# Kernel tuning notes

Measured on AMD Instinct MI355X. Metric: run time of the kernel, lower is better.

Reference implementation:

```python
import jax, jax.numpy as jnp
import numpy as np

B, T, C, H, N = 2, 1024, 2048, 32, 64  # batch, seq, n_embd==dim_att, heads, head_size
EPS_GN = 64e-5  # torch GroupNorm eps=0.00064


def setup_inputs() -> dict:
    key = jax.random.key(0)
    ks = jax.random.split(key, 40)
    def rn(i, shape, s):
        return jax.random.normal(ks[i], shape, dtype=jnp.float32) * s
    return {
        'x': jax.random.normal(ks[0], (B, T, C), dtype=jnp.float32),
        'shift_state': jnp.zeros((B, C), jnp.float32),
        'wkv_state': jnp.zeros((B, H, N, N), jnp.float32),
        'time_maa_x': rn(1, (1, 1, C), 0.3),
        'time_maa_rg': rn(2, (1, 1, C), 0.3),
        'time_maa_wa': rn(3, (1, 1, C), 0.3),
        'time_maa_k': rn(4, (1, 1, C), 0.3),
        'time_maa_v': rn(5, (1, 1, C), 0.3),
        'time_maa_w1': rn(6, (C, 128), 0.02),   # D_MIX_LORA*4 = 128
        'time_maa_w2': rn(7, (4, 32, C), 0.02),
        'time_decay': rn(8, (1, 1, C), 0.5) - 4.0,
        'time_decay_w1': rn(9, (C, 64), 0.02),
        'time_decay_w2': rn(10, (64, C), 0.02),
        'time_faaaa': rn(11, (1, 1, H, N), 0.02),
        'time_aaaaa': rn(12, (1, 1, C), 0.02),
        'time_aaa_w1': rn(13, (C, 16), 0.02),
        'time_aaa_w2': rn(14, (16, C), 0.02),
        'time_kkk_w1': rn(15, (C, 16), 0.02),
        'time_kkk_w2': rn(16, (16, C), 0.02),
        'gate_w1': rn(17, (C, 128), 0.02),
        'gate_w2': rn(18, (128, C), 0.02),
        'ma_w1': rn(19, (C, 16), 0.02),
        'ma_w2': rn(20, (16, C), 0.02),
        'time_misc_a': rn(21, (1, 1, C), 0.02),
        'mk_w1': rn(22, (C, 16), 0.02),
        'mk_w2': rn(23, (16, C), 0.02),
        'time_misc_k': rn(24, (1, 1, C), 0.02),
        'Wr': rn(25, (C, C), 0.5 / np.sqrt(C)),
        'Wk': rn(26, (C, C), 0.05 / np.sqrt(C)),
        'Wv': rn(27, (C, C), 0.5 / np.sqrt(C)),
        'Wo': rn(28, (C, C), 0.5 / np.sqrt(C)),
        'ln_w': jnp.ones((C,), jnp.float32),
        'ln_b': jnp.zeros((C,), jnp.float32),
    }


def _forward(x, shift_state, wkv_state, time_maa_x, time_maa_rg, time_maa_wa,
             time_maa_k, time_maa_v, time_maa_w1, time_maa_w2, time_decay,
             time_decay_w1, time_decay_w2, time_faaaa, time_aaaaa, time_aaa_w1,
             time_aaa_w2, time_kkk_w1, time_kkk_w2, gate_w1, gate_w2, ma_w1,
             ma_w2, time_misc_a, mk_w1, mk_w2, time_misc_k, Wr, Wk, Wv, Wo,
             ln_w, ln_b):
    # token shift difference
    xx = jnp.concatenate([shift_state[:, None, :], x[:, :-1]], axis=1) - x
    xmx = x + xx * time_maa_x
    m = jnp.tanh(xmx @ time_maa_w1).reshape(B, T, 4, -1)   # [B,T,4,32]
    m = jnp.einsum('btfd,fdc->fbtc', m, time_maa_w2)       # [4,B,T,C]
    mrg, mwa, mkm, mv = m[0], m[1], m[2], m[3]
    xrg = x + xx * (time_maa_rg + mrg)
    xwa = x + xx * (time_maa_wa + mwa)
    xk = x + xx * (time_maa_k + mkm)
    xv = x + xx * (time_maa_v + mv)
    r = xrg @ Wr.T
    w = -jax.nn.softplus(-(time_decay + jnp.tanh(xwa @ time_decay_w1) @ time_decay_w2)) - 0.5
    k = xk @ Wk.T
    v = xv @ Wv.T
    g = jnp.tanh(xrg @ gate_w1) @ gate_w2
    kk = k + jnp.tanh(xk @ time_kkk_w1) @ time_kkk_w2
    kkh = kk.reshape(B, T, H, N)
    nrm = jnp.maximum(jnp.linalg.norm(kkh, axis=-1, keepdims=True), 1e-12)  # F.normalize
    kk = (kkh / nrm).reshape(B, T, C)
    a = jax.nn.sigmoid(time_aaaaa + xwa @ time_aaa_w1 @ time_aaa_w2)
    ma = jax.nn.sigmoid(time_misc_a + xwa @ ma_w1 @ ma_w2)
    k = k * ma + k * a * (1.0 - ma)
    mk = jax.nn.sigmoid(time_misc_k + xk @ mk_w1 @ mk_w2)
    k = k * jnp.exp(jnp.minimum(w * mk, 0.0))  # clamp(w*mk, max=0).exp()

    # RWKV-7 recurrence (fused_recurrent_rwkv7 with a=-kk, b=kk*a_gate):
    #   S_t = diag(exp(w_t)) S_{t-1} + b_t (a_t^T S_{t-1}) + k_t v_t^T,  o_t = S_t^T r_t
    def heads(t):
        return jnp.moveaxis(t.reshape(B, T, H, N), 1, 0)  # [T,B,H,N]
    rs, ksq, vs, ws = heads(r), heads(k), heads(v), heads(w)
    a_s, b_s = heads(-kk), heads(kk * a)

    def step(S, inputs):  # S: [B,H,N_key,N_val]
        r_t, k_t, v_t, w_t, a_t, b_t = inputs
        sa = jnp.einsum('bhk,bhkv->bhv', a_t, S)
        S = S * jnp.exp(w_t)[..., None] + k_t[..., None] * v_t[..., None, :] + b_t[..., None] * sa[..., None, :]
        o = jnp.einsum('bhk,bhkv->bhv', r_t, S)
        return S, o

    S_final, o = jax.lax.scan(step, wkv_state, (rs, ksq, vs, ws, a_s, b_s))
    out = jnp.moveaxis(o, 0, 1).reshape(B, T, C)

    # GroupNorm(n_head groups, eps=64e-5), biased variance per head
    y = out.reshape(B * T, H, N)
    mu = y.mean(-1, keepdims=True)
    var = ((y - mu) ** 2).mean(-1, keepdims=True)
    y = (y - mu) / jnp.sqrt(var + EPS_GN)
    y = y * ln_w.reshape(H, N) + ln_b.reshape(H, N)
    xo = y.reshape(B, T, C)

    rh = r.reshape(B, T, H, N)
    kh = k.reshape(B, T, H, N)
    vh = v.reshape(B, T, H, N)
    xo = xo + ((rh * kh * time_faaaa).sum(-1, keepdims=True) * vh).reshape(B, T, C)
    xo = (xo * g) @ Wo.T
    return xo, x[:, -1], S_final


def reference(x, shift_state, wkv_state, time_maa_x, time_maa_rg, time_maa_wa,
              time_maa_k, time_maa_v, time_maa_w1, time_maa_w2, time_decay,
              time_decay_w1, time_decay_w2, time_faaaa, time_aaaaa, time_aaa_w1,
              time_aaa_w2, time_kkk_w1, time_kkk_w2, gate_w1, gate_w2, ma_w1,
              ma_w2, time_misc_a, mk_w1, mk_w2, time_misc_k, Wr, Wk, Wv, Wo,
              ln_w, ln_b):
    return _forward(x, shift_state, wkv_state, time_maa_x, time_maa_rg, time_maa_wa,
                    time_maa_k, time_maa_v, time_maa_w1, time_maa_w2, time_decay,
                    time_decay_w1, time_decay_w2, time_faaaa, time_aaaaa, time_aaa_w1,
                    time_aaa_w2, time_kkk_w1, time_kkk_w2, gate_w1, gate_w2, ma_w1,
                    ma_w2, time_misc_a, mk_w1, mk_w2, time_misc_k, Wr, Wk, Wv, Wo,
                    ln_w, ln_b)
```

## Files before the change

kernel.cpp:

```cpp
#include <hip/hip_runtime.h>
#include <hip/hip_bf16.h>
#include <math.h>


#define B_ 2
#define T_ 1024
#define C_ 2048
#define H_ 32
#define BT_ (B_*T_)
#define BTC_ ((size_t)BT_*C_)
#define CC_ ((size_t)C_*C_)
#define KS_ 8
#define CH_ 8

typedef __bf16 bf16x8 __attribute__((ext_vector_type(8)));
typedef float f32x4 __attribute__((ext_vector_type(4)));

__device__ __forceinline__ float wave64_sum(float v){
#pragma unroll
  for (int d = 1; d < 64; d <<= 1) v += __shfl_xor(v, d, 64);
  return v;
}

__device__ __forceinline__ float dpp_add_xor1(float x){
  int j = __builtin_amdgcn_mov_dpp(__float_as_int(x), 0xB1, 0xF, 0xF, true);
  return x + __int_as_float(j);
}
__device__ __forceinline__ float dpp_add_xor2(float x){
  int j = __builtin_amdgcn_mov_dpp(__float_as_int(x), 0x4E, 0xF, 0xF, true);
  return x + __int_as_float(j);
}
__device__ __forceinline__ float dpp_add_hmir(float x){
  int j = __builtin_amdgcn_mov_dpp(__float_as_int(x), 0x141, 0xF, 0xF, true);
  return x + __int_as_float(j);
}
__device__ __forceinline__ float dpp_add_mir(float x){
  int j = __builtin_amdgcn_mov_dpp(__float_as_int(x), 0x140, 0xF, 0xF, true);
  return x + __int_as_float(j);
}

__device__ __forceinline__ float red16(float x){
  x = dpp_add_xor1(x);
  x = dpp_add_xor2(x);
  x = dpp_add_hmir(x);
  x = dpp_add_mir(x);
  return x;
}

__device__ __forceinline__ size_t bhtn_idx(int r, int c){
  return (((size_t)(r >> 10)*H_ + (c >> 6))*T_ + (r & 1023))*64 + (c & 63);
}

__device__ __forceinline__ void gload_lds16(const float* g, float* l){
  __builtin_amdgcn_global_load_lds((const __attribute__((address_space(1))) void*)g,
                                   (__attribute__((address_space(3))) void*)l, 16, 0, 0);
}
__device__ __forceinline__ void gload_lds16b(const __hip_bfloat16* g, __bf16* l){
  __builtin_amdgcn_global_load_lds((const __attribute__((address_space(1))) void*)g,
                                   (__attribute__((address_space(3))) void*)l, 16, 0, 0);
}

__global__ __launch_bounds__(256) void f2bf_kernel(const float* __restrict__ in,
                                                   __hip_bfloat16* __restrict__ out, size_t n){
  size_t i = (size_t)blockIdx.x*256 + threadIdx.x;
  if (i < n) out[i] = __float2bfloat16(in[i]);
}

__global__ __launch_bounds__(256) void shift_kernel(const float* __restrict__ x,
                                                    const float* __restrict__ shift,
                                                    const float* __restrict__ maa_x,
                                                    float* __restrict__ xx, __hip_bfloat16* __restrict__ xmx_h){
  size_t idx = (size_t)blockIdx.x*256 + threadIdx.x;
  int c = (int)(idx % C_);
  size_t bt = idx / C_;
  int t = (int)(bt % T_);
  int b = (int)(bt / T_);
  float xv = x[idx];
  float prev = (t == 0) ? shift[(size_t)b*C_ + c] : x[idx - C_];
  float d = prev - xv;
  xx[idx] = d;
  xmx_h[idx] = __float2bfloat16(xv + d * maa_x[c]);
}

__global__ __launch_bounds__(256) void tp_pack(const float* __restrict__ in, __hip_bfloat16* __restrict__ out,
                                               int Nsrc, int row_off){
  __shared__ float tile[32][33];
  const int t = threadIdx.x;
  const int k0 = blockIdx.x*32, n0 = blockIdx.y*32;
  const int tn = t & 31, tk = t >> 5;
#pragma unroll
  for (int q = 0; q < 4; q++){
    int ki = tk + 8*q;
    float v = (n0 + tn < Nsrc) ? in[(size_t)(k0+ki)*Nsrc + n0 + tn] : 0.f;
    tile[tn][ki] = v;
  }
  __syncthreads();
#pragma unroll
  for (int q = 0; q < 4; q++){
    int no = tk + 8*q;
    if (n0 + no < Nsrc)
      out[(size_t)(row_off + n0 + no)*2048 + k0 + tn] = __float2bfloat16(tile[no][tn]);
  }
}

__global__ __launch_bounds__(256) void gemm_sk(const __hip_bfloat16* __restrict__ Ah,
                                               const __hip_bfloat16* __restrict__ Bh,
                                               float* __restrict__ parts, int K, int KC){
  __shared__ __bf16 As[128*32];
  __shared__ __bf16 Bs[128*32];
  const int tid = threadIdx.x;
  const int bm = blockIdx.x*128;
  const int z = blockIdx.y;
  const int wid = tid >> 6, lane = tid & 63;
  const int wr = (wid >> 1)*64, wc = (wid & 1)*64;
  const int fr = lane & 15, kg = lane >> 4;
  const int srow = tid >> 2, sk = (tid & 3)*8;
  __bf16* lA = As + wid*512;
  __bf16* lB = Bs + wid*512;
  f32x4 acc[4][4] = {};
  const int kend = z*KC + KC;
  for (int kt = z*KC; kt < kend; kt += 32){
    __syncthreads();
    gload_lds16b(Ah + (size_t)(bm+srow)*K + kt + sk,    lA);
    gload_lds16b(Ah + (size_t)(bm+srow+64)*K + kt + sk, lA + 64*32);
    gload_lds16b(Bh + (size_t)(srow)*K + kt + sk,       lB);
    gload_lds16b(Bh + (size_t)(srow+64)*K + kt + sk,    lB + 64*32);
    __builtin_amdgcn_s_waitcnt(0x3F70);
    __syncthreads();
    bf16x8 af[4], bfr[4];
#pragma unroll
    for (int i = 0; i < 4; i++){
      af[i]  = *(const bf16x8*)(As + (wr + i*16 + fr)*32 + kg*8);
      bfr[i] = *(const bf16x8*)(Bs + (wc + i*16 + fr)*32 + kg*8);
    }
#pragma unroll
    for (int mi = 0; mi < 4; mi++)
#pragma unroll
      for (int ni = 0; ni < 4; ni++)
        acc[mi][ni] = __builtin_amdgcn_mfma_f32_16x16x32_bf16(af[mi], bfr[ni], acc[mi][ni], 0, 0, 0);
  }
  float* Cc = parts + (size_t)z*BT_*128;
  const int orow0 = bm + wr + kg*4;
  const int ocol0 = wc + fr;
#pragma unroll
  for (int mi = 0; mi < 4; mi++)
#pragma unroll
    for (int ni = 0; ni < 4; ni++)
#pragma unroll
      for (int j = 0; j < 4; j++)
        Cc[(size_t)(orow0 + mi*16 + j)*128 + ocol0 + ni*16] = acc[mi][ni][j];
}

__global__ __launch_bounds__(256) void reduce_sk(const float* __restrict__ parts, float* __restrict__ out,
                                                 int tanh_lo, int tanh_hi){
  size_t idx = (size_t)blockIdx.x*256 + threadIdx.x;
  float s = 0.f;
#pragma unroll
  for (int z = 0; z < KS_; z++) s += parts[(size_t)z*BT_*128 + idx];
  int c = (int)(idx & 127);
  if (c >= tanh_lo && c < tanh_hi) s = tanhf(s);
  out[idx] = s;
}

__global__ __launch_bounds__(256) void mm_sk_g(const float* __restrict__ A, const float* __restrict__ W,
                                               __hip_bfloat16* __restrict__ out, int K){
  const int j = blockIdx.y*256 + threadIdx.x;
  const int i0 = blockIdx.x*8;
  float acc[8] = {0,0,0,0,0,0,0,0};
  for (int k = 0; k < K; k++){
    float wv = W[(size_t)k*C_ + j];
#pragma unroll
    for (int r = 0; r < 8; r++) acc[r] += A[(size_t)(i0+r)*K + k] * wv;
  }
#pragma unroll
  for (int r = 0; r < 8; r++) out[(size_t)(i0+r)*C_ + j] = __float2bfloat16(acc[r]);
}

__global__ __launch_bounds__(256) void mix_kernel(
    const float* __restrict__ m1, const float* __restrict__ w2,
    const float* __restrict__ x, const float* __restrict__ xx,
    const float* __restrict__ maa_rg, const float* __restrict__ maa_wa,
    const float* __restrict__ maa_k, const float* __restrict__ maa_v,
    __hip_bfloat16* __restrict__ xrg_h, __hip_bfloat16* __restrict__ xwa_h,
    __hip_bfloat16* __restrict__ xk_h, __hip_bfloat16* __restrict__ xv_h)
{
  const int j = blockIdx.y*256 + threadIdx.x;
  const int i0 = blockIdx.x*8;
  float acc[4][8] = {};
#pragma unroll
  for (int f = 0; f < 4; f++){
    for (int d = 0; d < 32; d++){
      float wv = w2[((size_t)f*32 + d)*C_ + j];
#pragma unroll
      for (int r = 0; r < 8; r++)
        acc[f][r] += m1[(size_t)(i0+r)*128 + f*32 + d] * wv;
    }
  }
  float mrg_ = maa_rg[j], mwa_ = maa_wa[j], mk_ = maa_k[j], mv_ = maa_v[j];
#pragma unroll
  for (int r = 0; r < 8; r++){
    size_t idx = (size_t)(i0+r)*C_ + j;
    float xval = x[idx], xxv = xx[idx];
    xrg_h[idx] = __float2bfloat16(xval + xxv*(mrg_ + acc[0][r]));
    xwa_h[idx] = __float2bfloat16(xval + xxv*(mwa_ + acc[1][r]));
    xk_h[idx]  = __float2bfloat16(xval + xxv*(mk_  + acc[2][r]));
    xv_h[idx]  = __float2bfloat16(xval + xxv*(mv_  + acc[3][r]));
  }
}

__global__ __launch_bounds__(256) void gemm_bt(const __hip_bfloat16* __restrict__ Ah,
                                               const __hip_bfloat16* __restrict__ Bh,
                                               float* __restrict__ Cc, int M, int Nn, int K){
  __shared__ __bf16 As[128*32];
  __shared__ __bf16 Bs[128*32];
  const int tid = threadIdx.x;
  const int bm = blockIdx.x*128, bn = blockIdx.y*128;
  const int wid = tid >> 6, lane = tid & 63;
  const int wr = (wid >> 1)*64, wc = (wid & 1)*64;
  const int fr = lane & 15, kg = lane >> 4;
  const int srow = tid >> 2, sk = (tid & 3)*8;
  __bf16* lA = As + wid*512;
  __bf16* lB = Bs + wid*512;
  f32x4 acc[4][4] = {};
  for (int kt = 0; kt < K; kt += 32){
    __syncthreads();
    gload_lds16b(Ah + (size_t)(bm+srow)*K + kt + sk,    lA);
    gload_lds16b(Ah + (size_t)(bm+srow+64)*K + kt + sk, lA + 64*32);
    gload_lds16b(Bh + (size_t)(bn+srow)*K + kt + sk,    lB);
    gload_lds16b(Bh + (size_t)(bn+srow+64)*K + kt + sk, lB + 64*32);
    __builtin_amdgcn_s_waitcnt(0x3F70);
    __syncthreads();
    bf16x8 af[4], bfr[4];
#pragma unroll
    for (int i = 0; i < 4; i++){
      af[i]  = *(const bf16x8*)(As + (wr + i*16 + fr)*32 + kg*8);
      bfr[i] = *(const bf16x8*)(Bs + (wc + i*16 + fr)*32 + kg*8);
    }
#pragma unroll
    for (int mi = 0; mi < 4; mi++)
#pragma unroll
      for (int ni = 0; ni < 4; ni++)
        acc[mi][ni] = __builtin_amdgcn_mfma_f32_16x16x32_bf16(af[mi], bfr[ni], acc[mi][ni], 0, 0, 0);
  }
  const int orow0 = bm + wr + kg*4;
  const int ocol0 = bn + wc + fr;
#pragma unroll
  for (int mi = 0; mi < 4; mi++)
#pragma unroll
    for (int ni = 0; ni < 4; ni++)
#pragma unroll
      for (int j = 0; j < 4; j++)
        Cc[(size_t)(orow0 + mi*16 + j)*Nn + ocol0 + ni*16] = acc[mi][ni][j];
}

__global__ __launch_bounds__(256) void gemm_bt_T(const __hip_bfloat16* __restrict__ Ah,
                                                 const __hip_bfloat16* __restrict__ Bh,
                                                 float* __restrict__ Cc, int K){
  __shared__ __bf16 As[128*32];
  __shared__ __bf16 Bs[128*32];
  const int tid = threadIdx.x;
  const int bm = blockIdx.x*128, bn = blockIdx.y*128;
  const int wid = tid >> 6, lane = tid & 63;
  const int wr = (wid >> 1)*64, wc = (wid & 1)*64;
  const int fr = lane & 15, kg = lane >> 4;
  const int srow = tid >> 2, sk = (tid & 3)*8;
  __bf16* lA = As + wid*512;
  __bf16* lB = Bs + wid*512;
  f32x4 acc[4][4] = {};
  for (int kt = 0; kt < K; kt += 32){
    __syncthreads();
    gload_lds16b(Ah + (size_t)(bm+srow)*K + kt + sk,    lA);
    gload_lds16b(Ah + (size_t)(bm+srow+64)*K + kt + sk, lA + 64*32);
    gload_lds16b(Bh + (size_t)(bn+srow)*K + kt + sk,    lB);
    gload_lds16b(Bh + (size_t)(bn+srow+64)*K + kt + sk, lB + 64*32);
    __builtin_amdgcn_s_waitcnt(0x3F70);
    __syncthreads();
    bf16x8 af[4], bfr[4];
#pragma unroll
    for (int i = 0; i < 4; i++){
      af[i]  = *(const bf16x8*)(As + (wr + i*16 + fr)*32 + kg*8);
      bfr[i] = *(const bf16x8*)(Bs + (wc + i*16 + fr)*32 + kg*8);
    }
#pragma unroll
    for (int mi = 0; mi < 4; mi++)
#pragma unroll
      for (int ni = 0; ni < 4; ni++)
        acc[mi][ni] = __builtin_amdgcn_mfma_f32_16x16x32_bf16(af[mi], bfr[ni], acc[mi][ni], 0, 0, 0);
  }
  const int r0 = bm + wr + kg*4;
  const int c0 = bn + wc + fr;
#pragma unroll
  for (int mi = 0; mi < 4; mi++)
#pragma unroll
    for (int ni = 0; ni < 4; ni++)
#pragma unroll
      for (int j = 0; j < 4; j++)
        Cc[bhtn_idx(r0 + mi*16 + j, c0 + ni*16)] = acc[mi][ni][j];
}

__global__ __launch_bounds__(256) void lora2_kernel(
    const float* __restrict__ wa1, const float* __restrict__ k1c,
    const float* __restrict__ dw2, const float* __restrict__ aw2, const float* __restrict__ maw2,
    const float* __restrict__ mkw2, const float* __restrict__ kkw2,
    const float* __restrict__ td, const float* __restrict__ aaaaa,
    const float* __restrict__ misc_a, const float* __restrict__ misc_k,
    float* __restrict__ k0, float* __restrict__ a_out,
    float* __restrict__ ew_out, float* __restrict__ kk0_out)
{
  const int j = blockIdx.y*256 + threadIdx.x;
  const int i0 = blockIdx.x*8;
  float accW[8] = {}, accA[8] = {}, accMA[8] = {}, accMK[8] = {}, accKK[8] = {};
  for (int k = 0; k < 64; k++){
    float wv = dw2[(size_t)k*C_ + j];
#pragma unroll
    for (int r = 0; r < 8; r++) accW[r] += wa1[(size_t)(i0+r)*128 + k] * wv;
  }
  for (int k = 0; k < 16; k++){
    float w_a  = aw2[(size_t)k*C_ + j];
    float w_ma = maw2[(size_t)k*C_ + j];
    float w_mk = mkw2[(size_t)k*C_ + j];
    float w_kk = kkw2[(size_t)k*C_ + j];
#pragma unroll
    for (int r = 0; r < 8; r++){
      accA[r]  += wa1[(size_t)(i0+r)*128 + 64 + k] * w_a;
      accMA[r] += wa1[(size_t)(i0+r)*128 + 80 + k] * w_ma;
      accKK[r] += k1c[(size_t)(i0+r)*128 + k] * w_kk;
      accMK[r] += k1c[(size_t)(i0+r)*128 + 16 + k] * w_mk;
    }
  }
  float tdv = td[j], aav = aaaaa[j], mav = misc_a[j], mkv = misc_k[j];
#pragma unroll
  for (int r = 0; r < 8; r++){
    size_t idx = bhtn_idx(i0+r, j);
    float u  = tdv + accW[r];
    float w  = -log1pf(expf(-u)) - 0.5f;
    float a  = 1.f/(1.f + expf(-(aav + accA[r])));
    float ma = 1.f/(1.f + expf(-(mav + accMA[r])));
    float mk = 1.f/(1.f + expf(-(mkv + accMK[r])));
    float kv = k0[idx];
    kk0_out[idx] = kv + accKK[r];
    float kn = kv * (ma + a*(1.f - ma)) * expf(fminf(w*mk, 0.f));
    k0[idx] = kn;
    a_out[idx] = a;
    ew_out[idx] = expf(w);
  }
}

__global__ __launch_bounds__(256) void kknorm_kernel(float* __restrict__ kk0, float* __restrict__ a_bs){
  const size_t grp = (size_t)blockIdx.x*4 + (threadIdx.x >> 6);
  const int lane = threadIdx.x & 63;
  const size_t idx = grp*64 + lane;
  float kv = kk0[idx];
  float ss = wave64_sum(kv*kv);
  float nrm = fmaxf(sqrtf(ss), 1e-12f);
  float kkn = kv / nrm;
  kk0[idx] = kkn;
  a_bs[idx] = kkn * a_bs[idx];
}

__global__ __launch_bounds__(64, 1) void rec_kernel(
    const float* __restrict__ rr, const float* __restrict__ kx,
    const float* __restrict__ vx, const float* __restrict__ ew,
    const float* __restrict__ kkv, const float* __restrict__ bsv,
    const float* __restrict__ s0, float* __restrict__ o, float* __restrict__ sT)
{
  __shared__ __align__(16) float lds[2][6][CH_*64];
  const int g = blockIdx.x;
  const int bh = g & 63;
  const int vg = g >> 6;
  const int b = bh >> 5, h = bh & 31;
  const int lane = threadIdx.x;
  const int cf = lane >> 4;
  const int kq = lane & 15;
  const int k0 = kq*4;
  const int v = vg*4 + cf;

  float S0, S1, S2, S3;
  {
    const float* p = s0 + ((size_t)bh*64 + k0)*64 + v;
    S0 = p[0]; S1 = p[64]; S2 = p[128]; S3 = p[192];
  }

  const size_t sb = (size_t)bh*T_*64;
  const float* g0 = kkv + sb;
  const float* g1 = ew  + sb;
  const float* g2 = kx  + sb;
  const float* g3 = bsv + sb;
  const float* g4 = rr  + sb;
  const float* g5 = vx  + sb;
  float* ob = o + (size_t)b*T_*C_ + h*64 + v;

#define STAGE(c, buf) do{ \
    const size_t co_ = (size_t)(c)*(CH_*64) + lane*4; \
    _Pragma("unroll") \
    for (int j_ = 0; j_ < 2; j_++){ \
      gload_lds16(g0 + co_ + j_*256, &lds[buf][0][j_*256]); \
      gload_lds16(g1 + co_ + j_*256, &lds[buf][1][j_*256]); \
      gload_lds16(g2 + co_ + j_*256, &lds[buf][2][j_*256]); \
      gload_lds16(g3 + co_ + j_*256, &lds[buf][3][j_*256]); \
      gload_lds16(g4 + co_ + j_*256, &lds[buf][4][j_*256]); \
      gload_lds16(g5 + co_ + j_*256, &lds[buf][5][j_*256]); \
    } }while(0)

  STAGE(0, 0);
  const int NCH = T_/CH_;
  for (int c = 0; c < NCH; c++){
    const int cn = (c+1 < NCH) ? c+1 : c;
    STAGE(cn, (c+1)&1);
    __builtin_amdgcn_s_waitcnt(0x0F7C);
    __builtin_amdgcn_sched_barrier(0);
    const int buf = c & 1;
#pragma unroll
    for (int s = 0; s < CH_; s++){
      const int so = s*64 + k0;
      const float4 A  = *(const float4*)(&lds[buf][0][so]);
      const float4 E  = *(const float4*)(&lds[buf][1][so]);
      const float4 Kk = *(const float4*)(&lds[buf][2][so]);
      const float4 Bv = *(const float4*)(&lds[buf][3][so]);
      const float4 R  = *(const float4*)(&lds[buf][4][so]);
      const float vt  = lds[buf][5][s*64 + v];
      float p = (A.x*S0 + A.y*S1) + (A.z*S2 + A.w*S3);
      p = red16(p);
      S0 = S0*E.x + Kk.x*vt - Bv.x*p;
      S1 = S1*E.y + Kk.y*vt - Bv.y*p;
      S2 = S2*E.z + Kk.z*vt - Bv.z*p;
      S3 = S3*E.w + Kk.w*vt - Bv.w*p;
      float op = (R.x*S0 + R.y*S1) + (R.z*S2 + R.w*S3);
      op = red16(op);
      if (kq == 0)
        ob[(size_t)(c*CH_ + s)*C_] = op;
    }
  }
#undef STAGE
  float* pT = sT + ((size_t)bh*64 + k0)*64 + v;
  pT[0] = S0; pT[64] = S1; pT[128] = S2; pT[192] = S3;
}

__global__ __launch_bounds__(256) void post_kernel(
    const float* __restrict__ o, const float* __restrict__ r, const float* __restrict__ k,
    const float* __restrict__ v, const __hip_bfloat16* __restrict__ g,
    const float* __restrict__ lnw, const float* __restrict__ lnb,
    const float* __restrict__ faaaa, __hip_bfloat16* __restrict__ z_h)
{
  const size_t grp = (size_t)blockIdx.x*4 + (threadIdx.x >> 6);
  const int lane = threadIdx.x & 63;
  const int h = (int)(grp & (H_-1));
  const int bt = (int)(grp >> 5);
  const size_t idx  = grp*64 + lane;
  const size_t idx2 = (((size_t)(bt >> 10)*H_ + h)*T_ + (bt & 1023))*64 + lane;
  const int ci = h*64 + lane;
  float y = o[idx];
  float mu = wave64_sum(y) * (1.f/64.f);
  float d = y - mu;
  float var = wave64_sum(d*d) * (1.f/64.f);
  float yn = d * rsqrtf(var + 64e-5f) * lnw[ci] + lnb[ci];
  float s = wave64_sum(r[idx2]*k[idx2]*faaaa[ci]);
  float xo = yn + s*v[idx2];
  z_h[idx] = __float2bfloat16(xo * __bfloat162float(g[idx]));
}

__global__ __launch_bounds__(256) void lastx_kernel(const float* __restrict__ x, float* __restrict__ out1){
  int idx = blockIdx.x*256 + threadIdx.x;
  int b = idx / C_, c = idx % C_;
  out1[idx] = x[((size_t)b*T_ + (T_-1))*C_ + c];
}

extern "C" void kernel_launch(void* const* d_in, const int* in_sizes, int n_in,
                              void* d_out, int out_size, void* d_ws, size_t ws_size,
                              hipStream_t stream){
  (void)in_sizes; (void)n_in; (void)out_size;
  const float* x      = (const float*)d_in[0];
  const float* shift  = (const float*)d_in[1];
  const float* wkv0   = (const float*)d_in[2];
  const float* maa_x  = (const float*)d_in[3];
  const float* maa_rg = (const float*)d_in[4];
  const float* maa_wa = (const float*)d_in[5];
  const float* maa_k  = (const float*)d_in[6];
  const float* maa_v  = (const float*)d_in[7];
  const float* maa_w1 = (const float*)d_in[8];
  const float* maa_w2 = (const float*)d_in[9];
  const float* tdecay = (const float*)d_in[10];
  const float* dw1    = (const float*)d_in[11];
  const float* dw2    = (const float*)d_in[12];
  const float* faaaa  = (const float*)d_in[13];
  const float* aaaaa  = (const float*)d_in[14];
  const float* aw1    = (const float*)d_in[15];
  const float* aw2    = (const float*)d_in[16];
  const float* kkw1   = (const float*)d_in[17];
  const float* kkw2   = (const float*)d_in[18];
  const float* gw1    = (const float*)d_in[19];
  const float* gw2    = (const float*)d_in[20];
  const float* maw1   = (const float*)d_in[21];
  const float* maw2   = (const float*)d_in[22];
  const float* misc_a = (const float*)d_in[23];
  const float* mkw1   = (const float*)d_in[24];
  const float* mkw2   = (const float*)d_in[25];
  const float* misc_k = (const float*)d_in[26];
  const float* Wr     = (const float*)d_in[27];
  const float* Wk     = (const float*)d_in[28];
  const float* Wv     = (const float*)d_in[29];
  const float* Wo     = (const float*)d_in[30];
  const float* lnw    = (const float*)d_in[31];
  const float* lnb    = (const float*)d_in[32];

  float* out0 = (float*)d_out;
  float* out1 = out0 + BTC_;
  float* outS = out1 + (size_t)B_*C_;

  const size_t NEEDED = (6*BTC_ + (size_t)3*BT_*128)*4 + 5*CC_*2 + (size_t)4*128*2048*2;
  if (ws_size < NEEDED) return;

  float* ws = (float*)d_ws;
  float* rbuf  = ws;
  float* kbuf  = ws + 1*BTC_;
  float* vbuf  = ws + 2*BTC_;
  float* abuf  = ws + 3*BTC_;
  float* ewbuf = ws + 4*BTC_;
  float* kkbuf = ws + 5*BTC_;
  float* xx    = abuf;
  float* wa1   = ws + 6*BTC_;
  float* g1f   = wa1 + (size_t)BT_*128;
  float* k1c   = g1f + (size_t)BT_*128;
  float* parts = rbuf;
  float* m1f   = vbuf;
  __hip_bfloat16* hb = (__hip_bfloat16*)(k1c + (size_t)BT_*128);
  __hip_bfloat16* xrg_h = hb;
  __hip_bfloat16* xwa_h = hb + 1*CC_;
  __hip_bfloat16* xk_h  = hb + 2*CC_;
  __hip_bfloat16* xv_h  = hb + 3*CC_;
  __hip_bfloat16* Wb    = hb + 4*CC_;
  __hip_bfloat16* WtB   = hb + 5*CC_;
  __hip_bfloat16* Wt_m  = WtB;
  __hip_bfloat16* Wt_wa = WtB + (size_t)128*2048;
  __hip_bfloat16* Wt_g  = WtB + (size_t)2*128*2048;
  __hip_bfloat16* Wt_k  = WtB + (size_t)3*128*2048;
  __hip_bfloat16* xmx_h = xv_h;
  __hip_bfloat16* g_h   = xwa_h;
  __hip_bfloat16* z_h   = xv_h;
  __hip_bfloat16* Wk_h  = (__hip_bfloat16*)ewbuf;
  __hip_bfloat16* Wv_h  = (__hip_bfloat16*)kkbuf;

  dim3 blk(256);
  const int KC = C_/KS_;

  hipMemsetAsync(WtB, 0, (size_t)4*128*2048*2, stream);
  tp_pack<<<dim3(64,4), blk, 0, stream>>>(maa_w1, Wt_m, 128, 0);
  tp_pack<<<dim3(64,2), blk, 0, stream>>>(dw1,  Wt_wa, 64, 0);
  tp_pack<<<dim3(64,1), blk, 0, stream>>>(aw1,  Wt_wa, 16, 64);
  tp_pack<<<dim3(64,1), blk, 0, stream>>>(maw1, Wt_wa, 16, 80);
  tp_pack<<<dim3(64,4), blk, 0, stream>>>(gw1,  Wt_g, 128, 0);
  tp_pack<<<dim3(64,1), blk, 0, stream>>>(kkw1, Wt_k, 16, 0);
  tp_pack<<<dim3(64,1), blk, 0, stream>>>(mkw1, Wt_k, 16, 16);

  shift_kernel<<<(int)(BTC_/256), blk, 0, stream>>>(x, shift, maa_x, xx, xmx_h);

  gemm_sk<<<dim3(BT_/128, KS_), blk, 0, stream>>>(xmx_h, Wt_m, parts, C_, KC);
  reduce_sk<<<BT_*128/256, blk, 0, stream>>>(parts, m1f, 0, 128);

  mix_kernel<<<dim3(BT_/8, C_/256), blk, 0, stream>>>(m1f, maa_w2, x, xx, maa_rg, maa_wa, maa_k, maa_v,
                                                      xrg_h, xwa_h, xk_h, xv_h);
  gemm_sk<<<dim3(BT_/128, KS_), blk, 0, stream>>>(xwa_h, Wt_wa, parts, C_, KC);
  reduce_sk<<<BT_*128/256, blk, 0, stream>>>(parts, wa1, 0, 64);
  gemm_sk<<<dim3(BT_/128, KS_), blk, 0, stream>>>(xrg_h, Wt_g, parts, C_, KC);
  reduce_sk<<<BT_*128/256, blk, 0, stream>>>(parts, g1f, 0, 128);
  gemm_sk<<<dim3(BT_/128, KS_), blk, 0, stream>>>(xk_h, Wt_k, parts, C_, KC);
  reduce_sk<<<BT_*128/256, blk, 0, stream>>>(parts, k1c, 0, 16);

  mm_sk_g<<<dim3(BT_/8, C_/256), blk, 0, stream>>>(g1f, gw2, g_h, 128);

  f2bf_kernel<<<(int)(CC_/256), blk, 0, stream>>>(Wr, Wb, CC_);
  f2bf_kernel<<<(int)(CC_/256), blk, 0, stream>>>(Wk, Wk_h, CC_);
  f2bf_kernel<<<(int)(CC_/256), blk, 0, stream>>>(Wv, Wv_h, CC_);
  gemm_bt_T<<<dim3(BT_/128, C_/128), blk, 0, stream>>>(xrg_h, Wb,   rbuf, C_);
  gemm_bt_T<<<dim3(BT_/128, C_/128), blk, 0, stream>>>(xk_h,  Wk_h, kbuf, C_);
  gemm_bt_T<<<dim3(BT_/128, C_/128), blk, 0, stream>>>(xv_h,  Wv_h, vbuf, C_);

  lora2_kernel<<<dim3(BT_/8, C_/256), blk, 0, stream>>>(wa1, k1c,
                                                        dw2, aw2, maw2, mkw2, kkw2,
                                                        tdecay, aaaaa, misc_a, misc_k,
                                                        kbuf, abuf, ewbuf, kkbuf);
  kknorm_kernel<<<BT_*H_/4, blk, 0, stream>>>(kkbuf, abuf);

  rec_kernel<<<1024, dim3(64), 0, stream>>>(rbuf, kbuf, vbuf, ewbuf, kkbuf, abuf, wkv0, out0, outS);

  post_kernel<<<BT_*H_/4, blk, 0, stream>>>(out0, rbuf, kbuf, vbuf, g_h, lnw, lnb, faaaa, z_h);
  f2bf_kernel<<<(int)(CC_/256), blk, 0, stream>>>(Wo, Wb, CC_);
  gemm_bt<<<dim3(BT_/128, C_/128), blk, 0, stream>>>(z_h, Wb, out0, BT_, C_, C_);
  lastx_kernel<<<(B_*C_)/256, blk, 0, stream>>>(x, out1);
}
```

Measured before the change: 862.6 us.

## Double-buffer LDS in GEMM kernels and batch r/k/v projections into one launch

The three MFMA GEMM kernels now use two LDS buffers, so the global-to-LDS load for the next K-tile is issued before the MFMAs on the current tile. This replaces two barriers per iteration with one, letting memory latency overlap compute. The three separate r/k/v projection GEMMs are merged into one launch that uses blockIdx.z to pick operands, which triples the grid and improves occupancy across CUs. In exchange LDS use doubles to 32KB per block, which may lower resident blocks per CU.

```diff
diff --git a/kernel.cpp b/kernel.cpp
--- a/kernel.cpp
+++ b/kernel.cpp
@@ -106,8 +106,8 @@
 __global__ __launch_bounds__(256) void gemm_sk(const __hip_bfloat16* __restrict__ Ah,
                                                const __hip_bfloat16* __restrict__ Bh,
                                                float* __restrict__ parts, int K, int KC){
-  __shared__ __bf16 As[128*32];
-  __shared__ __bf16 Bs[128*32];
+  __shared__ __bf16 As[2][128*32];
+  __shared__ __bf16 Bs[2][128*32];
   const int tid = threadIdx.x;
   const int bm = blockIdx.x*128;
   const int z = blockIdx.y;
@@ -115,30 +115,39 @@
   const int wr = (wid >> 1)*64, wc = (wid & 1)*64;
   const int fr = lane & 15, kg = lane >> 4;
   const int srow = tid >> 2, sk = (tid & 3)*8;
-  __bf16* lA = As + wid*512;
-  __bf16* lB = Bs + wid*512;
   f32x4 acc[4][4] = {};
   const int kend = z*KC + KC;
+#define SK_STAGE(kt_, b_) do{ \
+    gload_lds16b(Ah + (size_t)(bm+srow)*K + (kt_) + sk,    As[b_] + wid*512); \
+    gload_lds16b(Ah + (size_t)(bm+srow+64)*K + (kt_) + sk, As[b_] + wid*512 + 64*32); \
+    gload_lds16b(Bh + (size_t)(srow)*K + (kt_) + sk,       Bs[b_] + wid*512); \
+    gload_lds16b(Bh + (size_t)(srow+64)*K + (kt_) + sk,    Bs[b_] + wid*512 + 64*32); \
+  }while(0)
+  SK_STAGE(z*KC, 0);
+  __builtin_amdgcn_s_waitcnt(0x3F70);
+  __builtin_amdgcn_s_barrier();
+  __builtin_amdgcn_sched_barrier(0);
+  int buf = 0;
   for (int kt = z*KC; kt < kend; kt += 32){
-    __syncthreads();
-    gload_lds16b(Ah + (size_t)(bm+srow)*K + kt + sk,    lA);
-    gload_lds16b(Ah + (size_t)(bm+srow+64)*K + kt + sk, lA + 64*32);
-    gload_lds16b(Bh + (size_t)(srow)*K + kt + sk,       lB);
-    gload_lds16b(Bh + (size_t)(srow+64)*K + kt + sk,    lB + 64*32);
-    __builtin_amdgcn_s_waitcnt(0x3F70);
-    __syncthreads();
+    if (kt + 32 < kend) SK_STAGE(kt+32, buf^1);
     bf16x8 af[4], bfr[4];
 #pragma unroll
     for (int i = 0; i < 4; i++){
-      af[i]  = *(const bf16x8*)(As + (wr + i*16 + fr)*32 + kg*8);
-      bfr[i] = *(const bf16x8*)(Bs + (wc + i*16 + fr)*32 + kg*8);
+      af[i]  = *(const bf16x8*)(As[buf] + (wr + i*16 + fr)*32 + kg*8);
+      bfr[i] = *(const bf16x8*)(Bs[buf] + (wc + i*16 + fr)*32 + kg*8);
     }
 #pragma unroll
     for (int mi = 0; mi < 4; mi++)
 #pragma unroll
       for (int ni = 0; ni < 4; ni++)
         acc[mi][ni] = __builtin_amdgcn_mfma_f32_16x16x32_bf16(af[mi], bfr[ni], acc[mi][ni], 0, 0, 0);
-  }
+    __builtin_amdgcn_sched_barrier(0);
+    __builtin_amdgcn_s_waitcnt(0x3F70);
+    __builtin_amdgcn_s_barrier();
+    __builtin_amdgcn_sched_barrier(0);
+    buf ^= 1;
+  }
+#undef SK_STAGE
   float* Cc = parts + (size_t)z*BT_*128;
   const int orow0 = bm + wr + kg*4;
   const int ocol0 = wc + fr;
@@ -211,37 +220,46 @@
 __global__ __launch_bounds__(256) void gemm_bt(const __hip_bfloat16* __restrict__ Ah,
                                                const __hip_bfloat16* __restrict__ Bh,
                                                float* __restrict__ Cc, int M, int Nn, int K){
-  __shared__ __bf16 As[128*32];
-  __shared__ __bf16 Bs[128*32];
+  __shared__ __bf16 As[2][128*32];
+  __shared__ __bf16 Bs[2][128*32];
   const int tid = threadIdx.x;
   const int bm = blockIdx.x*128, bn = blockIdx.y*128;
   const int wid = tid >> 6, lane = tid & 63;
   const int wr = (wid >> 1)*64, wc = (wid & 1)*64;
   const int fr = lane & 15, kg = lane >> 4;
   const int srow = tid >> 2, sk = (tid & 3)*8;
-  __bf16* lA = As + wid*512;
-  __bf16* lB = Bs + wid*512;
   f32x4 acc[4][4] = {};
+#define BT_STAGE(kt_, b_) do{ \
+    gload_lds16b(Ah + (size_t)(bm+srow)*K + (kt_) + sk,    As[b_] + wid*512); \
+    gload_lds16b(Ah + (size_t)(bm+srow+64)*K + (kt_) + sk, As[b_] + wid*512 + 64*32); \
+    gload_lds16b(Bh + (size_t)(bn+srow)*K + (kt_) + sk,    Bs[b_] + wid*512); \
+    gload_lds16b(Bh + (size_t)(bn+srow+64)*K + (kt_) + sk, Bs[b_] + wid*512 + 64*32); \
+  }while(0)
+  BT_STAGE(0, 0);
+  __builtin_amdgcn_s_waitcnt(0x3F70);
+  __builtin_amdgcn_s_barrier();
+  __builtin_amdgcn_sched_barrier(0);
+  int buf = 0;
   for (int kt = 0; kt < K; kt += 32){
-    __syncthreads();
-    gload_lds16b(Ah + (size_t)(bm+srow)*K + kt + sk,    lA);
-    gload_lds16b(Ah + (size_t)(bm+srow+64)*K + kt + sk, lA + 64*32);
-    gload_lds16b(Bh + (size_t)(bn+srow)*K + kt + sk,    lB);
-    gload_lds16b(Bh + (size_t)(bn+srow+64)*K + kt + sk, lB + 64*32);
-    __builtin_amdgcn_s_waitcnt(0x3F70);
-    __syncthreads();
+    if (kt + 32 < K) BT_STAGE(kt+32, buf^1);
     bf16x8 af[4], bfr[4];
 #pragma unroll
     for (int i = 0; i < 4; i++){
-      af[i]  = *(const bf16x8*)(As + (wr + i*16 + fr)*32 + kg*8);
-      bfr[i] = *(const bf16x8*)(Bs + (wc + i*16 + fr)*32 + kg*8);
+      af[i]  = *(const bf16x8*)(As[buf] + (wr + i*16 + fr)*32 + kg*8);
+      bfr[i] = *(const bf16x8*)(Bs[buf] + (wc + i*16 + fr)*32 + kg*8);
     }
 #pragma unroll
     for (int mi = 0; mi < 4; mi++)
 #pragma unroll
       for (int ni = 0; ni < 4; ni++)
         acc[mi][ni] = __builtin_amdgcn_mfma_f32_16x16x32_bf16(af[mi], bfr[ni], acc[mi][ni], 0, 0, 0);
-  }
+    __builtin_amdgcn_sched_barrier(0);
+    __builtin_amdgcn_s_waitcnt(0x3F70);
+    __builtin_amdgcn_s_barrier();
+    __builtin_amdgcn_sched_barrier(0);
+    buf ^= 1;
+  }
+#undef BT_STAGE
   const int orow0 = bm + wr + kg*4;
   const int ocol0 = bn + wc + fr;
 #pragma unroll
@@ -253,40 +271,57 @@
         Cc[(size_t)(orow0 + mi*16 + j)*Nn + ocol0 + ni*16] = acc[mi][ni][j];
 }
 
-__global__ __launch_bounds__(256) void gemm_bt_T(const __hip_bfloat16* __restrict__ Ah,
-                                                 const __hip_bfloat16* __restrict__ Bh,
-                                                 float* __restrict__ Cc, int K){
-  __shared__ __bf16 As[128*32];
-  __shared__ __bf16 Bs[128*32];
+__global__ __launch_bounds__(256) void gemm_bt_T3(
+    const __hip_bfloat16* __restrict__ A0, const __hip_bfloat16* __restrict__ A1,
+    const __hip_bfloat16* __restrict__ A2,
+    const __hip_bfloat16* __restrict__ B0, const __hip_bfloat16* __restrict__ B1,
+    const __hip_bfloat16* __restrict__ B2,
+    float* __restrict__ C0, float* __restrict__ C1, float* __restrict__ C2, int K)
+{
+  __shared__ __bf16 As[2][128*32];
+  __shared__ __bf16 Bs[2][128*32];
+  const int zi = blockIdx.z;
+  const __hip_bfloat16* Ah = (zi == 0) ? A0 : (zi == 1) ? A1 : A2;
+  const __hip_bfloat16* Bh = (zi == 0) ? B0 : (zi == 1) ? B1 : B2;
+  float* Cc = (zi == 0) ? C0 : (zi == 1) ? C1 : C2;
   const int tid = threadIdx.x;
   const int bm = blockIdx.x*128, bn = blockIdx.y*128;
   const int wid = tid >> 6, lane = tid & 63;
   const int wr = (wid >> 1)*64, wc = (wid & 1)*64;
   const int fr = lane & 15, kg = lane >> 4;
   const int srow = tid >> 2, sk = (tid & 3)*8;
-  __bf16* lA = As + wid*512;
-  __bf16* lB = Bs + wid*512;
   f32x4 acc[4][4] = {};
+#define T3_STAGE(kt_, b_) do{ \
+    gload_lds16b(Ah + (size_t)(bm+srow)*K + (kt_) + sk,    As[b_] + wid*512); \
+    gload_lds16b(Ah + (size_t)(bm+srow+64)*K + (kt_) + sk, As[b_] + wid*512 + 64*32); \
+    gload_lds16b(Bh + (size_t)(bn+srow)*K + (kt_) + sk,    Bs[b_] + wid*512); \
+    gload_lds16b(Bh + (size_t)(bn+srow+64)*K + (kt_) + sk, Bs[b_] + wid*512 + 64*32); \
+  }while(0)
+  T3_STAGE(0, 0);
+  __builtin_amdgcn_s_waitcnt(0x3F70);
+  __builtin_amdgcn_s_barrier();
+  __builtin_amdgcn_sched_barrier(0);
+  int buf = 0;
   for (int kt = 0; kt < K; kt += 32){
-    __syncthreads();
-    gload_lds16b(Ah + (size_t)(bm+srow)*K + kt + sk,    lA);
-    gload_lds16b(Ah + (size_t)(bm+srow+64)*K + kt + sk, lA + 64*32);
-    gload_lds16b(Bh + (size_t)(bn+srow)*K + kt + sk,    lB);
-    gload_lds16b(Bh + (size_t)(bn+srow+64)*K + kt + sk, lB + 64*32);
-    __builtin_amdgcn_s_waitcnt(0x3F70);
-    __syncthreads();
+    if (kt + 32 < K) T3_STAGE(kt+32, buf^1);
     bf16x8 af[4], bfr[4];
 #pragma unroll
     for (int i = 0; i < 4; i++){
-      af[i]  = *(const bf16x8*)(As + (wr + i*16 + fr)*32 + kg*8);
-      bfr[i] = *(const bf16x8*)(Bs + (wc + i*16 + fr)*32 + kg*8);
+      af[i]  = *(const bf16x8*)(As[buf] + (wr + i*16 + fr)*32 + kg*8);
+      bfr[i] = *(const bf16x8*)(Bs[buf] + (wc + i*16 + fr)*32 + kg*8);
     }
 #pragma unroll
     for (int mi = 0; mi < 4; mi++)
 #pragma unroll
       for (int ni = 0; ni < 4; ni++)
         acc[mi][ni] = __builtin_amdgcn_mfma_f32_16x16x32_bf16(af[mi], bfr[ni], acc[mi][ni], 0, 0, 0);
-  }
+    __builtin_amdgcn_sched_barrier(0);
+    __builtin_amdgcn_s_waitcnt(0x3F70);
+    __builtin_amdgcn_s_barrier();
+    __builtin_amdgcn_sched_barrier(0);
+    buf ^= 1;
+  }
+#undef T3_STAGE
   const int r0 = bm + wr + kg*4;
   const int c0 = bn + wc + fr;
 #pragma unroll
@@ -571,9 +606,9 @@
   f2bf_kernel<<<(int)(CC_/256), blk, 0, stream>>>(Wr, Wb, CC_);
   f2bf_kernel<<<(int)(CC_/256), blk, 0, stream>>>(Wk, Wk_h, CC_);
   f2bf_kernel<<<(int)(CC_/256), blk, 0, stream>>>(Wv, Wv_h, CC_);
-  gemm_bt_T<<<dim3(BT_/128, C_/128), blk, 0, stream>>>(xrg_h, Wb,   rbuf, C_);
-  gemm_bt_T<<<dim3(BT_/128, C_/128), blk, 0, stream>>>(xk_h,  Wk_h, kbuf, C_);
-  gemm_bt_T<<<dim3(BT_/128, C_/128), blk, 0, stream>>>(xv_h,  Wv_h, vbuf, C_);
+  gemm_bt_T3<<<dim3(BT_/128, C_/128, 3), blk, 0, stream>>>(xrg_h, xk_h, xv_h,
+                                                           Wb, Wk_h, Wv_h,
+                                                           rbuf, kbuf, vbuf, C_);
 
   lora2_kernel<<<dim3(BT_/8, C_/256), blk, 0, stream>>>(wa1, k1c,
                                                         dw2, aw2, maw2, mkw2, kkw2,
```

New measurement: 771.9 us. 1.12x faster.
